# Kernel tuning notes

Measured on AMD Instinct MI355X. Metric: run time of the kernel, lower is better.

The kernel has to match this reference:

```python
import jax, jax.numpy as jnp
import numpy as np

N_TRACK = 50000
N_LANE = 50000
N_ATT = N_TRACK + N_LANE
NP_T = 1000000
NP_L = 500000
E_ATT = 1600000
D_TRACK = 4
D_LANE = 2
D_ATT = 10
HEADS = 30
D_OUT = 2
EPS = 1e-5
NEG_SLOPE = 0.2


def _mlp(x, W, b, g, beta):
    # Linear -> LayerNorm -> ReLU (matches MLP module)
    h = x @ W + b
    mu = h.mean(-1, keepdims=True)
    var = ((h - mu) ** 2).mean(-1, keepdims=True)
    h = (h - mu) * jax.lax.rsqrt(var + EPS) * g + beta
    return jax.nn.relu(h)


def _seg_max0(x, ids, n):
    # DGL max-reduce; nodes with no in-edges get 0
    m = jax.ops.segment_max(x, ids, num_segments=n, indices_are_sorted=True)
    return jnp.where(jnp.isfinite(m), m, 0.0)


def setup_inputs() -> dict:
    key = jax.random.key(0)
    ks = jax.random.split(key, 16)
    g = lambda i, shape, s=1.0: jax.random.normal(ks[i], shape, jnp.float32) * s
    return {
        'track_point_feats': g(0, (NP_T, D_TRACK)),
        'lane_point_feats': g(1, (NP_L, D_LANE)),
        'point_track_id': jnp.sort(jax.random.randint(ks[2], (NP_T,), 0, N_TRACK)),
        'point_lane_id': jnp.sort(jax.random.randint(ks[3], (NP_L,), 0, N_LANE)),
        'att_src': jax.random.randint(ks[4], (E_ATT,), 0, N_ATT),
        'att_dst': jnp.sort(jax.random.randint(ks[5], (E_ATT,), 0, N_ATT)),
        'track_mlp_W': g(6, (D_TRACK, D_TRACK), 0.5),
        'track_mlp_b': jnp.zeros((D_TRACK,), jnp.float32),
        'track_ln_g': jnp.ones((D_TRACK,), jnp.float32),
        'track_ln_b': jnp.zeros((D_TRACK,), jnp.float32),
        'track_out_W': g(7, (D_TRACK, D_ATT), 0.5),
        'track_out_b': jnp.zeros((D_ATT,), jnp.float32),
        'lane_mlp_W': g(8, (D_LANE, D_LANE), 0.5),
        'lane_mlp_b': jnp.zeros((D_LANE,), jnp.float32),
        'lane_ln_g': jnp.ones((D_LANE,), jnp.float32),
        'lane_ln_b': jnp.zeros((D_LANE,), jnp.float32),
        'lane_out_W': g(9, (D_LANE, D_ATT), 0.5),
        'lane_out_b': jnp.zeros((D_ATT,), jnp.float32),
        'gat_fc_W': g(10, (D_ATT, HEADS * D_OUT), 0.3),
        'gat_attn_l': g(11, (HEADS, D_OUT), 0.3),
        'gat_attn_r': g(12, (HEADS, D_OUT), 0.3),
        'gat_bias': jnp.zeros((HEADS * D_OUT,), jnp.float32),
    }


def reference(track_point_feats, lane_point_feats, point_track_id, point_lane_id,
              att_src, att_dst,
              track_mlp_W, track_mlp_b, track_ln_g, track_ln_b, track_out_W, track_out_b,
              lane_mlp_W, lane_mlp_b, lane_ln_g, lane_ln_b, lane_out_W, lane_out_b,
              gat_fc_W, gat_attn_l, gat_attn_r, gat_bias):
    # SubTrackModel: per-point MLP -> segment max over point->track -> linear
    track_pool = _seg_max0(_mlp(track_point_feats, track_mlp_W, track_mlp_b, track_ln_g, track_ln_b),
                           point_track_id, N_TRACK)
    track_feats = track_pool @ track_out_W + track_out_b  # [N_TRACK, 10]
    # SubLaneModel
    lane_pool = _seg_max0(_mlp(lane_point_feats, lane_mlp_W, lane_mlp_b, lane_ln_g, lane_ln_b),
                          point_lane_id, N_LANE)
    lane_feats = lane_pool @ lane_out_W + lane_out_b  # [N_LANE, 10]
    feats = jnp.concatenate([track_feats, lane_feats], axis=0)  # [N_ATT, 10]

    # GATConv (30 heads, out 2)
    h = (feats @ gat_fc_W).reshape(N_ATT, HEADS, D_OUT)
    el = jnp.einsum('nhd,hd->nh', h, gat_attn_l)
    er = jnp.einsum('nhd,hd->nh', h, gat_attn_r)
    e = jax.nn.leaky_relu(el[att_src] + er[att_dst], NEG_SLOPE)  # [E, H]
    m = jax.ops.segment_max(e, att_dst, num_segments=N_ATT, indices_are_sorted=True)
    m = jnp.where(jnp.isfinite(m), m, 0.0)
    ee = jnp.exp(e - m[att_dst])
    den = jax.ops.segment_sum(ee, att_dst, num_segments=N_ATT, indices_are_sorted=True)
    alpha = ee / den[att_dst]  # edge softmax over incoming edges per dst
    msg = alpha[:, :, None] * h[att_src]  # [E, H, D_OUT]
    out = jax.ops.segment_sum(msg, att_dst, num_segments=N_ATT, indices_are_sorted=True)
    out = out.reshape(N_ATT, HEADS * D_OUT) + gat_bias
    return out[:N_TRACK]
```

## Files before the change

### kernel.cpp

```cpp
#include <hip/hip_runtime.h>
#include <hip/hip_bf16.h>
#include <math.h>

#define N_TRACK 50000
#define N_LANE  50000
#define N_ATT   (N_TRACK + N_LANE)
#define NP_T    1000000
#define NP_L    500000
#define E_ATT   1600000
#define HEADS   30
#define EPS     1e-5f
#define NEG_SLOPE 0.2f

typedef __attribute__((ext_vector_type(4))) float nfloat4;
typedef __attribute__((ext_vector_type(2))) float nfloat2;

#define REC_DW 32

__global__ void point_kernel(const nfloat4* __restrict__ xt, const nfloat2* __restrict__ xl,
                             const int* __restrict__ idt, const int* __restrict__ idl,
                             const float* __restrict__ tW, const float* __restrict__ tb,
                             const float* __restrict__ tg, const float* __restrict__ tbeta,
                             const float* __restrict__ lW, const float* __restrict__ lb,
                             const float* __restrict__ lg, const float* __restrict__ lbeta,
                             float* __restrict__ pool_t, float* __restrict__ pool_l) {
    int tid = blockIdx.x * blockDim.x + threadIdx.x;
    int lane = threadIdx.x & 63;
    int id = -1;
    float y0 = 0.f, y1 = 0.f, y2 = 0.f, y3 = 0.f;
    if (tid < NP_T) {
        nfloat4 xv = __builtin_nontemporal_load(&xt[tid]);
        float h[4];
        #pragma unroll
        for (int j = 0; j < 4; j++)
            h[j] = xv.x * tW[0*4+j] + xv.y * tW[1*4+j] + xv.z * tW[2*4+j] + xv.w * tW[3*4+j] + tb[j];
        float mu = 0.25f * (h[0] + h[1] + h[2] + h[3]);
        float var = 0.f;
        #pragma unroll
        for (int j = 0; j < 4; j++) { float d = h[j] - mu; var += d * d; }
        var *= 0.25f;
        float r = rsqrtf(var + EPS);
        y0 = fmaxf((h[0] - mu) * r * tg[0] + tbeta[0], 0.f);
        y1 = fmaxf((h[1] - mu) * r * tg[1] + tbeta[1], 0.f);
        y2 = fmaxf((h[2] - mu) * r * tg[2] + tbeta[2], 0.f);
        y3 = fmaxf((h[3] - mu) * r * tg[3] + tbeta[3], 0.f);
        id = __builtin_nontemporal_load(&idt[tid]);
    } else if (tid < NP_T + NP_L) {
        int t = tid - NP_T;
        nfloat2 xv = __builtin_nontemporal_load(&xl[t]);
        float h0 = xv.x * lW[0] + xv.y * lW[2] + lb[0];
        float h1 = xv.x * lW[1] + xv.y * lW[3] + lb[1];
        float mu = 0.5f * (h0 + h1);
        float var = 0.5f * ((h0 - mu) * (h0 - mu) + (h1 - mu) * (h1 - mu));
        float r = rsqrtf(var + EPS);
        y0 = fmaxf((h0 - mu) * r * lg[0] + lbeta[0], 0.f);
        y1 = fmaxf((h1 - mu) * r * lg[1] + lbeta[1], 0.f);
        id = N_TRACK + __builtin_nontemporal_load(&idl[t]);
    }
    #pragma unroll
    for (int d = 1; d < 64; d <<= 1) {
        int oid = __shfl_down(id, d, 64);
        float o0 = __shfl_down(y0, d, 64);
        float o1 = __shfl_down(y1, d, 64);
        float o2 = __shfl_down(y2, d, 64);
        float o3 = __shfl_down(y3, d, 64);
        if (oid == id) {
            y0 = fmaxf(y0, o0); y1 = fmaxf(y1, o1);
            y2 = fmaxf(y2, o2); y3 = fmaxf(y3, o3);
        }
    }
    int pid = __shfl_up(id, 1, 64);
    bool head = (lane == 0) || (pid != id);
    if (id >= 0 && head) {
        if (id < N_TRACK) {
            unsigned int* p = (unsigned int*)&pool_t[(size_t)id * 4];
            atomicMax(p + 0, __float_as_uint(y0));
            atomicMax(p + 1, __float_as_uint(y1));
            atomicMax(p + 2, __float_as_uint(y2));
            atomicMax(p + 3, __float_as_uint(y3));
        } else {
            unsigned int* p = (unsigned int*)&pool_l[(size_t)(id - N_TRACK) * 2];
            atomicMax(p + 0, __float_as_uint(y0));
            atomicMax(p + 1, __float_as_uint(y1));
        }
    }
}

__global__ void node_kernel(const float* __restrict__ pool_t, const float* __restrict__ pool_l,
                            const float* __restrict__ tW, const float* __restrict__ tb,
                            const float* __restrict__ lW, const float* __restrict__ lb,
                            const float* __restrict__ fcW,
                            const int* __restrict__ att_dst,
                            unsigned int* __restrict__ hpack, int* __restrict__ off) {
    int i = blockIdx.x * blockDim.x + threadIdx.x;

    if (i <= N_TRACK) {
        int lo = 0, hi = E_ATT;
        while (lo < hi) {
            int mid = (lo + hi) >> 1;
            if (att_dst[mid] < i) lo = mid + 1; else hi = mid;
        }
        off[i] = lo;
    }
    if (i >= N_ATT) return;

    float f[10];
    if (i < N_TRACK) {
        const float4 p = *(const float4*)(pool_t + (size_t)i * 4);
        #pragma unroll
        for (int j = 0; j < 10; j++)
            f[j] = p.x * tW[0*10+j] + p.y * tW[1*10+j] + p.z * tW[2*10+j] + p.w * tW[3*10+j] + tb[j];
    } else {
        const float2 p = *(const float2*)(pool_l + (size_t)(i - N_TRACK) * 2);
        #pragma unroll
        for (int j = 0; j < 10; j++)
            f[j] = p.x * lW[0*10+j] + p.y * lW[1*10+j] + lb[j];
    }

    unsigned int rec[REC_DW];
    #pragma unroll
    for (int hh = 0; hh < HEADS; hh++) {
        float a0 = 0.f, a1 = 0.f;
        #pragma unroll
        for (int k = 0; k < 10; k++) {
            a0 += f[k] * fcW[k * 60 + 2 * hh];
            a1 += f[k] * fcW[k * 60 + 2 * hh + 1];
        }
        unsigned int b0 = (unsigned int)__hip_bfloat16_raw(__float2bfloat16(a0)).x;
        unsigned int b1 = (unsigned int)__hip_bfloat16_raw(__float2bfloat16(a1)).x;
        rec[hh] = b0 | (b1 << 16);
    }
    rec[30] = 0u; rec[31] = 0u;

    uint4* rp = (uint4*)(hpack + (size_t)i * REC_DW);
    #pragma unroll
    for (int q = 0; q < 8; q++)
        rp[q] = make_uint4(rec[4*q], rec[4*q+1], rec[4*q+2], rec[4*q+3]);
}

__global__ void edge_kernel(const int* __restrict__ src, const int* __restrict__ off,
                            const unsigned int* __restrict__ hpack,
                            const float* __restrict__ attn_l, const float* __restrict__ attn_r,
                            const float* __restrict__ bias, float* __restrict__ out) {
    int grp = blockIdx.x * 8 + (threadIdx.x >> 5);
    int hh = threadIdx.x & 31;
    if (grp >= N_TRACK || hh >= HEADS) return;

    float al0 = attn_l[2 * hh], al1 = attn_l[2 * hh + 1];
    float ar0 = attn_r[2 * hh], ar1 = attn_r[2 * hh + 1];

    unsigned int dd = hpack[(size_t)grp * REC_DW + hh];
    float er = __uint_as_float(dd << 16) * ar0 + __uint_as_float(dd & 0xffff0000u) * ar1;

    int s = off[grp], e = off[grp + 1];
    float m = -INFINITY;
    float den_a = 0.f, n0_a = 0.f, n1_a = 0.f;
    float den_b = 0.f, n0_b = 0.f, n1_b = 0.f;

    for (int kk = s; kk < e; kk += 16) {
        int sv[16];
        #pragma unroll
        for (int j = 0; j < 16; j++) sv[j] = src[kk + j < e ? kk + j : kk];
        unsigned int d[16];
        #pragma unroll
        for (int j = 0; j < 16; j++) d[j] = hpack[(size_t)sv[j] * REC_DW + hh];

        float h0[16], h1[16], ev[16];
        #pragma unroll
        for (int j = 0; j < 16; j++) {
            h0[j] = __uint_as_float(d[j] << 16);
            h1[j] = __uint_as_float(d[j] & 0xffff0000u);
            float x = h0[j] * al0 + h1[j] * al1 + er;
            x = (x > 0.f) ? x : NEG_SLOPE * x;
            ev[j] = (kk + j < e) ? x : -INFINITY;
        }
        float mx[8];
        #pragma unroll
        for (int j = 0; j < 8; j++) mx[j] = fmaxf(ev[j], ev[j + 8]);
        #pragma unroll
        for (int j = 0; j < 4; j++) mx[j] = fmaxf(mx[j], mx[j + 4]);
        float bm = fmaxf(fmaxf(mx[0], mx[1]), fmaxf(mx[2], mx[3]));

        float nm = fmaxf(m, bm);
        float sc = (m > -INFINITY) ? __expf(m - nm) : 0.f;
        den_a *= sc; n0_a *= sc; n1_a *= sc;
        den_b *= sc; n0_b *= sc; n1_b *= sc;
        m = nm;
        #pragma unroll
        for (int j = 0; j < 16; j += 2) {
            float wa = __expf(ev[j] - nm);
            float wb = __expf(ev[j + 1] - nm);
            den_a += wa;            den_b += wb;
            n0_a += wa * h0[j];     n0_b += wb * h0[j + 1];
            n1_a += wa * h1[j];     n1_b += wb * h1[j + 1];
        }
    }

    float den = den_a + den_b, n0 = n0_a + n0_b, n1 = n1_a + n1_b;
    float o0 = 0.f, o1 = 0.f;
    if (den > 0.f) {
        float inv = 1.f / den;
        o0 = n0 * inv; o1 = n1 * inv;
    }
    nfloat2 v = { o0 + bias[2 * hh], o1 + bias[2 * hh + 1] };
    __builtin_nontemporal_store(v, (nfloat2*)out + (size_t)grp * HEADS + hh);
}

extern "C" void kernel_launch(void* const* d_in, const int* in_sizes, int n_in,
                              void* d_out, int out_size, void* d_ws, size_t ws_size,
                              hipStream_t stream) {
    const nfloat4* track_pts = (const nfloat4*)d_in[0];
    const nfloat2* lane_pts  = (const nfloat2*)d_in[1];
    const int* pt_track_id  = (const int*)d_in[2];
    const int* pt_lane_id   = (const int*)d_in[3];
    const int* att_src      = (const int*)d_in[4];
    const int* att_dst      = (const int*)d_in[5];
    const float* track_mlp_W = (const float*)d_in[6];
    const float* track_mlp_b = (const float*)d_in[7];
    const float* track_ln_g  = (const float*)d_in[8];
    const float* track_ln_b  = (const float*)d_in[9];
    const float* track_out_W = (const float*)d_in[10];
    const float* track_out_b = (const float*)d_in[11];
    const float* lane_mlp_W  = (const float*)d_in[12];
    const float* lane_mlp_b  = (const float*)d_in[13];
    const float* lane_ln_g   = (const float*)d_in[14];
    const float* lane_ln_b   = (const float*)d_in[15];
    const float* lane_out_W  = (const float*)d_in[16];
    const float* lane_out_b  = (const float*)d_in[17];
    const float* gat_fc_W    = (const float*)d_in[18];
    const float* gat_attn_l  = (const float*)d_in[19];
    const float* gat_attn_r  = (const float*)d_in[20];
    const float* gat_bias    = (const float*)d_in[21];
    float* out = (float*)d_out;

    float* pool_t = (float*)d_ws;
    float* pool_l = pool_t + 200000;
    int*   off    = (int*)(pool_l + 100000);
    unsigned int* hpack = (unsigned int*)(off + 50016);

    (void)hipMemsetAsync(d_ws, 0, 300000 * sizeof(float), stream);

    point_kernel<<<(NP_T + NP_L + 255) / 256, 256, 0, stream>>>(
        track_pts, lane_pts, pt_track_id, pt_lane_id,
        track_mlp_W, track_mlp_b, track_ln_g, track_ln_b,
        lane_mlp_W, lane_mlp_b, lane_ln_g, lane_ln_b,
        pool_t, pool_l);
    node_kernel<<<(N_ATT + 255) / 256, 256, 0, stream>>>(
        pool_t, pool_l, track_out_W, track_out_b, lane_out_W, lane_out_b,
        gat_fc_W, att_dst, hpack, off);
    edge_kernel<<<(N_TRACK + 7) / 8, 256, 0, stream>>>(
        att_src, off, hpack, gat_attn_l, gat_attn_r, gat_bias, out);
}
```

Baseline: 171.1 us.

## Process two points per thread and build CSR offsets via boundary scan in point kernel

The point kernel now handles two consecutive points per thread, merging their results locally before the wave-level segmented max, which halves the thread count and the shuffle work per point. CSR offsets for destination nodes are no longer found with a per-node binary search in the node kernel. Instead each point thread scans two edges, detects changes in the sorted destination ids, and writes the offsets there. The cost is an extra read of att_dst inside the point kernel and more registers per thread.

```diff
diff --git a/kernel.cpp b/kernel.cpp
--- a/kernel.cpp
+++ b/kernel.cpp
@@ -17,46 +17,113 @@
 
 #define REC_DW 32
 
+#define PT_THREADS 800000
+
 __global__ void point_kernel(const nfloat4* __restrict__ xt, const nfloat2* __restrict__ xl,
                              const int* __restrict__ idt, const int* __restrict__ idl,
                              const float* __restrict__ tW, const float* __restrict__ tb,
                              const float* __restrict__ tg, const float* __restrict__ tbeta,
                              const float* __restrict__ lW, const float* __restrict__ lb,
                              const float* __restrict__ lg, const float* __restrict__ lbeta,
-                             float* __restrict__ pool_t, float* __restrict__ pool_l) {
-    int tid = blockIdx.x * blockDim.x + threadIdx.x;
+                             const int* __restrict__ att_dst,
+                             float* __restrict__ pool_t, float* __restrict__ pool_l,
+                             int* __restrict__ off) {
+    int t = blockIdx.x * blockDim.x + threadIdx.x;
+    if (t >= PT_THREADS) return;
     int lane = threadIdx.x & 63;
+
+    #pragma unroll
+    for (int r = 0; r < 2; r++) {
+        int eix = t + r * PT_THREADS;
+        int d1 = att_dst[eix];
+        int d0 = (eix == 0) ? -1 : att_dst[eix - 1];
+        int jmax = (d1 < N_TRACK) ? d1 : N_TRACK;
+        for (int j = d0 + 1; j <= jmax; j++) off[j] = eix;
+        if (eix == E_ATT - 1)
+            for (int j = d1 + 1; j <= N_TRACK; j++) off[j] = E_ATT;
+    }
+
     int id = -1;
     float y0 = 0.f, y1 = 0.f, y2 = 0.f, y3 = 0.f;
-    if (tid < NP_T) {
-        nfloat4 xv = __builtin_nontemporal_load(&xt[tid]);
-        float h[4];
-        #pragma unroll
-        for (int j = 0; j < 4; j++)
-            h[j] = xv.x * tW[0*4+j] + xv.y * tW[1*4+j] + xv.z * tW[2*4+j] + xv.w * tW[3*4+j] + tb[j];
-        float mu = 0.25f * (h[0] + h[1] + h[2] + h[3]);
-        float var = 0.f;
-        #pragma unroll
-        for (int j = 0; j < 4; j++) { float d = h[j] - mu; var += d * d; }
-        var *= 0.25f;
-        float r = rsqrtf(var + EPS);
-        y0 = fmaxf((h[0] - mu) * r * tg[0] + tbeta[0], 0.f);
-        y1 = fmaxf((h[1] - mu) * r * tg[1] + tbeta[1], 0.f);
-        y2 = fmaxf((h[2] - mu) * r * tg[2] + tbeta[2], 0.f);
-        y3 = fmaxf((h[3] - mu) * r * tg[3] + tbeta[3], 0.f);
-        id = __builtin_nontemporal_load(&idt[tid]);
-    } else if (tid < NP_T + NP_L) {
-        int t = tid - NP_T;
-        nfloat2 xv = __builtin_nontemporal_load(&xl[t]);
-        float h0 = xv.x * lW[0] + xv.y * lW[2] + lb[0];
-        float h1 = xv.x * lW[1] + xv.y * lW[3] + lb[1];
-        float mu = 0.5f * (h0 + h1);
-        float var = 0.5f * ((h0 - mu) * (h0 - mu) + (h1 - mu) * (h1 - mu));
-        float r = rsqrtf(var + EPS);
-        y0 = fmaxf((h0 - mu) * r * lg[0] + lbeta[0], 0.f);
-        y1 = fmaxf((h1 - mu) * r * lg[1] + lbeta[1], 0.f);
-        id = N_TRACK + __builtin_nontemporal_load(&idl[t]);
-    }
+
+    if (t < NP_T / 2) {
+        nfloat4 xv0 = __builtin_nontemporal_load(&xt[2 * t]);
+        nfloat4 xv1 = __builtin_nontemporal_load(&xt[2 * t + 1]);
+        float ya[4], yb[4];
+        {
+            float h[4];
+            #pragma unroll
+            for (int j = 0; j < 4; j++)
+                h[j] = xv0.x * tW[0*4+j] + xv0.y * tW[1*4+j] + xv0.z * tW[2*4+j] + xv0.w * tW[3*4+j] + tb[j];
+            float mu = 0.25f * (h[0] + h[1] + h[2] + h[3]);
+            float var = 0.f;
+            #pragma unroll
+            for (int j = 0; j < 4; j++) { float d = h[j] - mu; var += d * d; }
+            float rr = rsqrtf(var * 0.25f + EPS);
+            #pragma unroll
+            for (int j = 0; j < 4; j++) ya[j] = fmaxf((h[j] - mu) * rr * tg[j] + tbeta[j], 0.f);
+        }
+        {
+            float h[4];
+            #pragma unroll
+            for (int j = 0; j < 4; j++)
+                h[j] = xv1.x * tW[0*4+j] + xv1.y * tW[1*4+j] + xv1.z * tW[2*4+j] + xv1.w * tW[3*4+j] + tb[j];
+            float mu = 0.25f * (h[0] + h[1] + h[2] + h[3]);
+            float var = 0.f;
+            #pragma unroll
+            for (int j = 0; j < 4; j++) { float d = h[j] - mu; var += d * d; }
+            float rr = rsqrtf(var * 0.25f + EPS);
+            #pragma unroll
+            for (int j = 0; j < 4; j++) yb[j] = fmaxf((h[j] - mu) * rr * tg[j] + tbeta[j], 0.f);
+        }
+        int2 ids = *(const int2*)&idt[2 * t];
+        if (ids.x == ids.y) {
+            yb[0] = fmaxf(yb[0], ya[0]); yb[1] = fmaxf(yb[1], ya[1]);
+            yb[2] = fmaxf(yb[2], ya[2]); yb[3] = fmaxf(yb[3], ya[3]);
+        } else {
+            unsigned int* p = (unsigned int*)&pool_t[(size_t)ids.x * 4];
+            atomicMax(p + 0, __float_as_uint(ya[0]));
+            atomicMax(p + 1, __float_as_uint(ya[1]));
+            atomicMax(p + 2, __float_as_uint(ya[2]));
+            atomicMax(p + 3, __float_as_uint(ya[3]));
+        }
+        id = ids.y;
+        y0 = yb[0]; y1 = yb[1]; y2 = yb[2]; y3 = yb[3];
+    } else if (t < NP_T / 2 + NP_L / 2) {
+        int u = t - NP_T / 2;
+        nfloat2 xv0 = __builtin_nontemporal_load(&xl[2 * u]);
+        nfloat2 xv1 = __builtin_nontemporal_load(&xl[2 * u + 1]);
+        float ya[2], yb[2];
+        {
+            float h0 = xv0.x * lW[0] + xv0.y * lW[2] + lb[0];
+            float h1 = xv0.x * lW[1] + xv0.y * lW[3] + lb[1];
+            float mu = 0.5f * (h0 + h1);
+            float var = 0.5f * ((h0 - mu) * (h0 - mu) + (h1 - mu) * (h1 - mu));
+            float rr = rsqrtf(var + EPS);
+            ya[0] = fmaxf((h0 - mu) * rr * lg[0] + lbeta[0], 0.f);
+            ya[1] = fmaxf((h1 - mu) * rr * lg[1] + lbeta[1], 0.f);
+        }
+        {
+            float h0 = xv1.x * lW[0] + xv1.y * lW[2] + lb[0];
+            float h1 = xv1.x * lW[1] + xv1.y * lW[3] + lb[1];
+            float mu = 0.5f * (h0 + h1);
+            float var = 0.5f * ((h0 - mu) * (h0 - mu) + (h1 - mu) * (h1 - mu));
+            float rr = rsqrtf(var + EPS);
+            yb[0] = fmaxf((h0 - mu) * rr * lg[0] + lbeta[0], 0.f);
+            yb[1] = fmaxf((h1 - mu) * rr * lg[1] + lbeta[1], 0.f);
+        }
+        int2 ids = *(const int2*)&idl[2 * u];
+        if (ids.x == ids.y) {
+            yb[0] = fmaxf(yb[0], ya[0]); yb[1] = fmaxf(yb[1], ya[1]);
+        } else {
+            unsigned int* p = (unsigned int*)&pool_l[(size_t)ids.x * 2];
+            atomicMax(p + 0, __float_as_uint(ya[0]));
+            atomicMax(p + 1, __float_as_uint(ya[1]));
+        }
+        id = N_TRACK + ids.y;
+        y0 = yb[0]; y1 = yb[1];
+    }
+
     #pragma unroll
     for (int d = 1; d < 64; d <<= 1) {
         int oid = __shfl_down(id, d, 64);
@@ -90,18 +157,8 @@
                             const float* __restrict__ tW, const float* __restrict__ tb,
                             const float* __restrict__ lW, const float* __restrict__ lb,
                             const float* __restrict__ fcW,
-                            const int* __restrict__ att_dst,
-                            unsigned int* __restrict__ hpack, int* __restrict__ off) {
+                            unsigned int* __restrict__ hpack) {
     int i = blockIdx.x * blockDim.x + threadIdx.x;
-
-    if (i <= N_TRACK) {
-        int lo = 0, hi = E_ATT;
-        while (lo < hi) {
-            int mid = (lo + hi) >> 1;
-            if (att_dst[mid] < i) lo = mid + 1; else hi = mid;
-        }
-        off[i] = lo;
-    }
     if (i >= N_ATT) return;
 
     float f[10];
@@ -240,14 +297,14 @@
 
     (void)hipMemsetAsync(d_ws, 0, 300000 * sizeof(float), stream);
 
-    point_kernel<<<(NP_T + NP_L + 255) / 256, 256, 0, stream>>>(
+    point_kernel<<<(PT_THREADS + 255) / 256, 256, 0, stream>>>(
         track_pts, lane_pts, pt_track_id, pt_lane_id,
         track_mlp_W, track_mlp_b, track_ln_g, track_ln_b,
         lane_mlp_W, lane_mlp_b, lane_ln_g, lane_ln_b,
-        pool_t, pool_l);
+        att_dst, pool_t, pool_l, off);
     node_kernel<<<(N_ATT + 255) / 256, 256, 0, stream>>>(
         pool_t, pool_l, track_out_W, track_out_b, lane_out_W, lane_out_b,
-        gat_fc_W, att_dst, hpack, off);
+        gat_fc_W, hpack);
     edge_kernel<<<(N_TRACK + 7) / 8, 256, 0, stream>>>(
         att_src, off, hpack, gat_attn_l, gat_attn_r, gat_bias, out);
 }
```

Result: slower. 174.6 us (+2.0%).
